# Kernel tuning notes

Measured on AMD Instinct MI355X. Metric: run time of the kernel, lower is better.

Reference implementation:

```python
import jax, jax.numpy as jnp
from jax import lax
import numpy as np

B, T, IN, H, L, C = 1024, 64, 64, 512, 8, 128


def setup_inputs() -> dict:
    key = jax.random.key(0)
    ks = jax.random.split(key, 11)
    s_in = 1.0 / np.sqrt(H)
    return {
        "x": jax.random.normal(ks[0], (B, T, IN), jnp.float32),
        "w_ih0": jax.random.normal(ks[1], (4 * H, IN), jnp.float32) * s_in,
        "w_hh0": jax.random.normal(ks[2], (4 * H, H), jnp.float32) * s_in,
        "b_ih0": jax.random.normal(ks[3], (4 * H,), jnp.float32) * s_in,
        "b_hh0": jax.random.normal(ks[4], (4 * H,), jnp.float32) * s_in,
        "w_ih": jax.random.normal(ks[5], (L - 1, 4 * H, H), jnp.float32) * s_in,
        "w_hh": jax.random.normal(ks[6], (L - 1, 4 * H, H), jnp.float32) * s_in,
        "b_ih": jax.random.normal(ks[7], (L - 1, 4 * H), jnp.float32) * s_in,
        "b_hh": jax.random.normal(ks[8], (L - 1, 4 * H), jnp.float32) * s_in,
        "fc_w": jax.random.normal(ks[9], (C, H * T), jnp.float32) * (1.0 / np.sqrt(H * T)),
        "fc_b": jax.random.normal(ks[10], (C,), jnp.float32) * 0.01,
    }


def _lstm_layer(x_tbd, wi, wh, bi, bh):
    # x_tbd: [T, B, D_in]; returns hidden sequence [T, B, H]
    b = x_tbd.shape[1]
    h_dim = wh.shape[1]
    bias = bi + bh

    def step(carry, x_t):
        h, c = carry
        gates = x_t @ wi.T + h @ wh.T + bias  # [B, 4H]
        i, f, g, o = jnp.split(gates, 4, axis=-1)  # PyTorch gate order i,f,g,o
        i = jax.nn.sigmoid(i)
        f = jax.nn.sigmoid(f)
        g = jnp.tanh(g)
        o = jax.nn.sigmoid(o)
        c = f * c + i * g
        h = o * jnp.tanh(c)
        return (h, c), h

    h0 = jnp.zeros((b, h_dim), x_tbd.dtype)
    _, hs = lax.scan(step, (h0, h0), x_tbd)
    return hs


def reference(x, w_ih0, w_hh0, b_ih0, b_hh0, w_ih, w_hh, b_ih, b_hh, fc_w, fc_b):
    xt = jnp.transpose(x, (1, 0, 2))  # [T, B, IN]
    h = _lstm_layer(xt, w_ih0, w_hh0, b_ih0, b_hh0)
    for l in range(w_ih.shape[0]):  # fixed small layer count
        h = _lstm_layer(h, w_ih[l], w_hh[l], b_ih[l], b_hh[l])
    out = jnp.transpose(h, (1, 0, 2)).reshape(x.shape[0], -1)  # [B, T*H]
    return out @ fc_w.T + fc_b
```

## Files before the change

kernel.cpp:

```cpp
#include <hip/hip_runtime.h>
#include <hip/hip_bf16.h>

#define BB   1024
#define TT   64
#define IND  64
#define HH   512
#define G4   2048
#define NLAYER 8
#define NCLS 128
#define KP   1024
#define RS   8
#define SLOT (32 * 1024 * 16)

typedef __bf16 bf16x8 __attribute__((ext_vector_type(8)));
typedef float  f32x4  __attribute__((ext_vector_type(4)));

typedef const __attribute__((address_space(1))) void* as1cvp;
typedef __attribute__((address_space(3))) void* as3vp;

__device__ __forceinline__ void gload16(void* lds, const void* g) {
  __builtin_amdgcn_global_load_lds((as1cvp)g, (as3vp)lds, 16, 0, 0);
}

__device__ __forceinline__ float sigmf(float x) { return 1.f / (1.f + __expf(-x)); }
__device__ __forceinline__ float tanhfast(float x) { return 2.f / (1.f + __expf(-2.f * x)) - 1.f; }

__global__ void cvt_kernel(const float* __restrict__ s, __bf16* __restrict__ d, int n) {
  int i = blockIdx.x * 256 + threadIdx.x;
  if (i < n) d[i] = (__bf16)s[i];
}

__global__ void pack_w(const float* __restrict__ whh0, const float* __restrict__ wih0,
                       const float* __restrict__ whh, const float* __restrict__ wih,
                       __bf16* __restrict__ Wp) {
  int i = blockIdx.x * 256 + threadIdx.x;
  int k = i & (KP - 1), n = (i >> 10) & 2047, l = i >> 21;
  float v;
  if (k < 512) v = (l == 0) ? whh0[n * 512 + k] : whh[((size_t)(l - 1) * G4 + n) * 512 + k];
  else if (l == 0) v = (k < 512 + IND) ? wih0[n * IND + (k - 512)] : 0.f;
  else v = wih[((size_t)(l - 1) * G4 + n) * 512 + (k - 512)];
  Wp[i] = (__bf16)v;
}

__global__ void bias_prep(const float* __restrict__ bi0, const float* __restrict__ bh0,
                          const float* __restrict__ bi, const float* __restrict__ bh,
                          float* __restrict__ biasb) {
  int i = blockIdx.x * 256 + threadIdx.x;
  int l = i >> 11, k = i & 2047;
  float v = (l == 0) ? (bi0[k] + bh0[k]) : (bi[(l - 1) * G4 + k] + bh[(l - 1) * G4 + k]);
  biasb[i] = v;
}

__global__ void zero_u32(unsigned* __restrict__ p, int n) {
  int i = blockIdx.x * 256 + threadIdx.x;
  if (i < n) p[i] = 0u;
}

__global__ __launch_bounds__(256, 2) void lstm_all(
    const float* __restrict__ xf,
    const __bf16* __restrict__ Wp,
    const float* __restrict__ biasb,
    __bf16* __restrict__ hring,
    __bf16* __restrict__ h7,
    unsigned* __restrict__ flags,
    unsigned* __restrict__ xslot) {
  extern __shared__ __bf16 Wlds[];
  __shared__ int sbs;
  const int tid = threadIdx.x;

  if (tid == 0) {
    unsigned xcc;
    asm volatile("s_getreg_b32 %0, hwreg(HW_REG_XCC_ID)" : "=s"(xcc));
    xcc &= 7u;
    unsigned slot = __hip_atomic_fetch_add(xslot + xcc, 1u, __ATOMIC_RELAXED,
                                           __HIP_MEMORY_SCOPE_AGENT) & 63u;
    sbs = (int)((xcc << 6) | slot);
  }
  __syncthreads();
  const int l  = sbs >> 6;
  const int bx = (sbs >> 5) & 1;
  const int by = sbs & 31;
  const int j0 = by << 4;
  const __bf16* Wl = Wp + (size_t)l * G4 * KP;

  for (int it = 0; it < 16; ++it) {
    const int p = it * 256 + tid;
    const int kt = p >> 8;
    const int q = p & 255;
    const int u = q >> 2;
    const int g = (q & 3) ^ ((u >> 1) & 3);
    const int n = ((u >> 4) << 9) + j0 + (u & 15);
    gload16(&Wlds[p * 8], Wl + (size_t)n * KP + kt * 32 + g * 8);
  }

  const int lane = tid & 63, wv = tid >> 6;
  const int qr = lane >> 4, ml = lane & 15;
  const __bf16* wb[4];
  float bv[4];
  int wsw[4];
#pragma unroll
  for (int g = 0; g < 4; ++g) {
    const int n = g * 512 + j0 + ml;
    wb[g] = Wl + (size_t)n * KP + 512 + qr * 8;
    bv[g] = biasb[l * G4 + n];
    const int u = g * 16 + ml;
    wsw[g] = u * 32 + ((qr ^ ((u >> 1) & 3)) << 3);
  }
  const int r0 = (bx << 9) + (wv << 7);
  const int rowA = r0 + ml;
  const int abase = ((qr >> 1) << 14) + rowA * 16 + ((qr & 1) << 3);
  __bf16* ringL = hring + (size_t)l * RS * SLOT;
  const __bf16* ringU = hring + (size_t)((l > 0 ? l : 1) - 1) * RS * SLOT;
  unsigned* ownf = flags + (l * 2 + bx) * 64;
  unsigned* upf  = flags + ((l > 0 ? l - 1 : 0) * 2 + bx) * 64;
  unsigned* dnf  = flags + ((l < 7 ? l + 1 : 7) * 2 + bx) * 64;
  float c8[8][4] = {};
  __syncthreads();

  for (int t = 0; t < TT; ++t) {
    if (wv == 0) {
      const bool isown = (lane < 32);
      const unsigned* fp = isown ? (ownf + lane) : (upf + (lane - 32));
      const unsigned need = isown ? (unsigned)t : (unsigned)(t + 1);
      const bool act = isown ? (t > 0) : (l > 0);
      for (;;) {
        unsigned v = act ? __hip_atomic_load(fp, __ATOMIC_RELAXED,
                                             __HIP_MEMORY_SCOPE_AGENT)
                         : need;
        if (__all((int)(v >= need))) break;
        __builtin_amdgcn_s_sleep(1);
      }
    }
    __syncthreads();
    if (t > 0 && (t & (RS - 1)) == 0)
      __builtin_amdgcn_fence(__ATOMIC_ACQUIRE, "agent");

    f32x4 acc[8][4];
#pragma unroll
    for (int m = 0; m < 8; ++m)
#pragma unroll
      for (int g = 0; g < 4; ++g)
#pragma unroll
        for (int r = 0; r < 4; ++r) acc[m][g][r] = bv[g];

    if (l == 0) {
#pragma unroll
      for (int m = 0; m < 8; ++m) {
        const float* xr = xf + ((size_t)(rowA + m * 16) * TT + t) * IND + qr * 8;
        const f32x4 f0 = *(const f32x4*)xr;
        const f32x4 f1 = *(const f32x4*)(xr + 4);
        const f32x4 f2 = *(const f32x4*)(xr + 32);
        const f32x4 f3 = *(const f32x4*)(xr + 36);
        bf16x8 a0, a1;
#pragma unroll
        for (int r = 0; r < 4; ++r) {
          a0[r] = (__bf16)f0[r]; a0[4 + r] = (__bf16)f1[r];
          a1[r] = (__bf16)f2[r]; a1[4 + r] = (__bf16)f3[r];
        }
#pragma unroll
        for (int g = 0; g < 4; ++g) {
          acc[m][g] = __builtin_amdgcn_mfma_f32_16x16x32_bf16(
              a0, *(const bf16x8*)(wb[g]), acc[m][g], 0, 0, 0);
          acc[m][g] = __builtin_amdgcn_mfma_f32_16x16x32_bf16(
              a1, *(const bf16x8*)(wb[g] + 32), acc[m][g], 0, 0, 0);
        }
      }
    } else {
      const __bf16* src = ringU + (size_t)(t & (RS - 1)) * SLOT + abase;
      bf16x8 A0[4], A1[4], Wr[2][4];
#pragma unroll
      for (int m = 0; m < 4; ++m) A0[m] = *(const bf16x8*)(src + m * 256);
#pragma unroll
      for (int m = 0; m < 4; ++m) A1[m] = *(const bf16x8*)(src + (4 + m) * 256);
#pragma unroll
      for (int g = 0; g < 4; ++g) Wr[0][g] = *(const bf16x8*)(wb[g]);
#pragma unroll
      for (int kt = 0; kt < 16; ++kt) {
        const __bf16* aknx = src + (kt + 1) * 32768;
#pragma unroll
        for (int m = 0; m < 4; ++m)
#pragma unroll
          for (int g = 0; g < 4; ++g)
            acc[m][g] = __builtin_amdgcn_mfma_f32_16x16x32_bf16(
                A0[m], Wr[kt & 1][g], acc[m][g], 0, 0, 0);
        if (kt < 15) {
#pragma unroll
          for (int m = 0; m < 4; ++m) A0[m] = *(const bf16x8*)(aknx + m * 256);
#pragma unroll
          for (int g = 0; g < 4; ++g)
            Wr[(kt + 1) & 1][g] = *(const bf16x8*)(wb[g] + (kt + 1) * 32);
        }
        __builtin_amdgcn_sched_barrier(0);
#pragma unroll
        for (int m = 0; m < 4; ++m)
#pragma unroll
          for (int g = 0; g < 4; ++g)
            acc[4 + m][g] = __builtin_amdgcn_mfma_f32_16x16x32_bf16(
                A1[m], Wr[kt & 1][g], acc[4 + m][g], 0, 0, 0);
        if (kt < 15) {
#pragma unroll
          for (int m = 0; m < 4; ++m) A1[m] = *(const bf16x8*)(aknx + (4 + m) * 256);
        }
        __builtin_amdgcn_sched_barrier(0);
      }
    }

    if (t > 0) {
      const __bf16* srcH = ((l < 7) ? ringL + (size_t)((t - 1) & (RS - 1)) * SLOT
                                    : h7 + (size_t)(t - 1) * SLOT) + abase;
      bf16x8 A0[4], A1[4];
#pragma unroll
      for (int m = 0; m < 4; ++m) A0[m] = *(const bf16x8*)(srcH + m * 256);
#pragma unroll
      for (int m = 0; m < 4; ++m) A1[m] = *(const bf16x8*)(srcH + (4 + m) * 256);
#pragma unroll
      for (int kt = 0; kt < 16; ++kt) {
        const __bf16* aknx = srcH + (kt + 1) * 32768;
        bf16x8 wf[4];
#pragma unroll
        for (int g = 0; g < 4; ++g) wf[g] = *(const bf16x8*)&Wlds[kt * 2048 + wsw[g]];
#pragma unroll
        for (int m = 0; m < 4; ++m)
#pragma unroll
          for (int g = 0; g < 4; ++g)
            acc[m][g] = __builtin_amdgcn_mfma_f32_16x16x32_bf16(
                A0[m], wf[g], acc[m][g], 0, 0, 0);
        if (kt < 15) {
#pragma unroll
          for (int m = 0; m < 4; ++m) A0[m] = *(const bf16x8*)(aknx + m * 256);
        }
        __builtin_amdgcn_sched_barrier(0);
#pragma unroll
        for (int m = 0; m < 4; ++m)
#pragma unroll
          for (int g = 0; g < 4; ++g)
            acc[4 + m][g] = __builtin_amdgcn_mfma_f32_16x16x32_bf16(
                A1[m], wf[g], acc[4 + m][g], 0, 0, 0);
        if (kt < 15) {
#pragma unroll
          for (int m = 0; m < 4; ++m) A1[m] = *(const bf16x8*)(aknx + (4 + m) * 256);
        }
        __builtin_amdgcn_sched_barrier(0);
      }
    }

    if (wv == 0 && l < 7 && t >= RS) {
      const unsigned need = (unsigned)(t - (RS - 1));
      for (;;) {
        unsigned v = (lane < 32) ? __hip_atomic_load(dnf + lane, __ATOMIC_RELAXED,
                                                     __HIP_MEMORY_SCOPE_AGENT)
                                 : need;
        if (__all((int)(v >= need))) break;
        __builtin_amdgcn_s_sleep(1);
      }
    }
    __syncthreads();

    unsigned short* dst = (unsigned short*)(((l < 7)
        ? ringL + (size_t)(t & (RS - 1)) * SLOT
        : h7 + (size_t)t * SLOT) + ((size_t)by << 14)) + ml;
#pragma unroll
    for (int m = 0; m < 8; ++m) {
      const int rbm = r0 + m * 16 + (qr << 2);
#pragma unroll
      for (int r = 0; r < 4; ++r) {
        const float gi = sigmf(acc[m][0][r]);
        const float gf = sigmf(acc[m][1][r]);
        const float gg = tanhfast(acc[m][2][r]);
        const float go = sigmf(acc[m][3][r]);
        const float cv = gf * c8[m][r] + gi * gg;
        c8[m][r] = cv;
        const __bf16 hv = (__bf16)(go * tanhfast(cv));
        __hip_atomic_store(dst + (size_t)(rbm + r) * 16,
                           __builtin_bit_cast(unsigned short, hv),
                           __ATOMIC_RELAXED, __HIP_MEMORY_SCOPE_AGENT);
      }
    }
    __syncthreads();
    if (tid == 0)
      __hip_atomic_store(ownf + by, (unsigned)(t + 1), __ATOMIC_RELAXED,
                         __HIP_MEMORY_SCOPE_AGENT);
  }
}

__global__ __launch_bounds__(256, 2) void fc_kernel(
    const __bf16* __restrict__ hseq, const __bf16* __restrict__ fcw,
    float* __restrict__ partial) {
  __shared__ __bf16 At[64 * 32];
  __shared__ __bf16 Wt[128 * 32];
  const int tid = threadIdx.x;
  const int b0 = blockIdx.x * 64;
  const int kbase = blockIdx.y * 2048;
  const int lane = tid & 63, wv = tid >> 6;
  const int qr = lane >> 4, ml = lane & 15;
  const int wr = (wv >> 1) * 32, wc = (wv & 1) * 64;
  const int sr = tid >> 2, sk = (tid & 3) * 8;

  f32x4 acc[2][4];
  for (int i = 0; i < 2; i++)
    for (int j = 0; j < 4; j++)
      for (int r = 0; r < 4; r++) acc[i][j][r] = 0.f;

  for (int kt = 0; kt < 64; ++kt) {
    const int k = kbase + kt * 32;
    const int t = k >> 9;
    const int kk = (k & 511) + sk;
    gload16(&At[tid * 8],
            hseq + (size_t)t * SLOT + ((size_t)(kk >> 4) * 1024 + b0 + sr) * 16 + (kk & 15));
    gload16(&Wt[tid * 8],        fcw + (size_t)sr * (TT * HH) + k + sk);
    gload16(&Wt[2048 + tid * 8], fcw + (size_t)(sr + 64) * (TT * HH) + k + sk);
    __syncthreads();
    bf16x8 af[2], bfr[4];
    for (int i = 0; i < 2; i++) af[i]  = *(const bf16x8*)&At[(wr + i * 16 + ml) * 32 + qr * 8];
    for (int j = 0; j < 4; j++) bfr[j] = *(const bf16x8*)&Wt[(wc + j * 16 + ml) * 32 + qr * 8];
    for (int i = 0; i < 2; i++)
      for (int j = 0; j < 4; j++)
        acc[i][j] = __builtin_amdgcn_mfma_f32_16x16x32_bf16(af[i], bfr[j], acc[i][j], 0, 0, 0);
    __syncthreads();
  }
  for (int i = 0; i < 2; i++)
    for (int j = 0; j < 4; j++)
      for (int r = 0; r < 4; r++)
        partial[((size_t)blockIdx.y * BB + b0 + wr + i * 16 + qr * 4 + r) * NCLS + wc + j * 16 + ml] =
            acc[i][j][r];
}

__global__ void fc_reduce(const float* __restrict__ partial, const float* __restrict__ fcb,
                          float* __restrict__ out) {
  int i = blockIdx.x * 256 + threadIdx.x;
  float s = fcb[i & 127];
  for (int p = 0; p < 16; p++) s += partial[(size_t)p * (BB * NCLS) + i];
  out[i] = s;
}

extern "C" void kernel_launch(void* const* d_in, const int* in_sizes, int n_in,
                              void* d_out, int out_size, void* d_ws, size_t ws_size,
                              hipStream_t stream) {
  const float* x    = (const float*)d_in[0];
  const float* wih0 = (const float*)d_in[1];
  const float* whh0 = (const float*)d_in[2];
  const float* bih0 = (const float*)d_in[3];
  const float* bhh0 = (const float*)d_in[4];
  const float* wih  = (const float*)d_in[5];
  const float* whh  = (const float*)d_in[6];
  const float* bih  = (const float*)d_in[7];
  const float* bhh  = (const float*)d_in[8];
  const float* fcw  = (const float*)d_in[9];
  const float* fcb  = (const float*)d_in[10];
  float* out = (float*)d_out;

  hipFuncSetAttribute((const void*)lstm_all,
                      hipFuncAttributeMaxDynamicSharedMemorySize, 65536);

  size_t off = 0;
  char* base = (char*)d_ws;
  auto carve = [&](size_t bytes) -> char* {
    char* p = base + off;
    off += (bytes + 255) & ~(size_t)255;
    return p;
  };
  __bf16*   Wp    = (__bf16*)carve((size_t)NLAYER * G4 * KP * 2);
  __bf16*   fcwb  = (__bf16*)carve((size_t)NCLS * TT * HH * 2);
  float*    biasb = (float*)carve((size_t)NLAYER * G4 * 4);
  __bf16*   hring = (__bf16*)carve((size_t)7 * RS * SLOT * 2);
  __bf16*   h7    = (__bf16*)carve((size_t)TT * SLOT * 2);
  float*    part  = (float*)carve((size_t)16 * BB * NCLS * 4);
  unsigned* flags = (unsigned*)carve((size_t)(NLAYER * 2 * 64 + 64) * 4);
  unsigned* xslot = flags + NLAYER * 2 * 64;

  pack_w<<<(NLAYER * G4 * KP) / 256, 256, 0, stream>>>(whh0, wih0, whh, wih, Wp);
  cvt_kernel<<<(NCLS * TT * HH) / 256, 256, 0, stream>>>(fcw, fcwb, NCLS * TT * HH);
  bias_prep<<<(NLAYER * G4) / 256, 256, 0, stream>>>(bih0, bhh0, bih, bhh, biasb);
  zero_u32<<<(NLAYER * 2 * 64 + 64 + 255) / 256, 256, 0, stream>>>(
      flags, NLAYER * 2 * 64 + 64);

  lstm_all<<<512, 256, 65536, stream>>>(x, Wp, biasb, hring, h7, flags, xslot);

  fc_kernel<<<dim3(16, 16), 256, 0, stream>>>(h7, fcwb, part);
  fc_reduce<<<(BB * NCLS) / 256, 256, 0, stream>>>(part, fcb, out);
}
```

Measured before the change: 4.292 ms.

## Compute next step's input projection before waiting on own-layer hidden state

Restructures the per-timestep loop so the input-to-hidden MFMA work for step t+1 runs right after publishing h_t, instead of after waiting for every peer block's h_t. The goal is to take the input projection off the recurrent critical path, so the wait on sibling blocks overlaps with useful work. The upstream-layer flag wait also moves to just before that early projection. This adds an extra barrier per step and changes the order of flag waits, which could shift pipeline dependencies between layers.

```diff
diff --git a/kernel.cpp b/kernel.cpp
--- a/kernel.cpp
+++ b/kernel.cpp
@@ -115,18 +115,143 @@
   unsigned* upf  = flags + ((l > 0 ? l - 1 : 0) * 2 + bx) * 64;
   unsigned* dnf  = flags + ((l < 7 ? l + 1 : 7) * 2 + bx) * 64;
   float c8[8][4] = {};
+  f32x4 acc[8][4];
   __syncthreads();
 
+  auto initAcc = [&]() {
+#pragma unroll
+    for (int m = 0; m < 8; ++m)
+#pragma unroll
+      for (int g = 0; g < 4; ++g)
+#pragma unroll
+        for (int r = 0; r < 4; ++r) acc[m][g][r] = bv[g];
+  };
+
+  auto xpartL0 = [&](int tx) {
+#pragma unroll
+    for (int m = 0; m < 8; ++m) {
+      const float* xr = xf + ((size_t)(rowA + m * 16) * TT + tx) * IND + qr * 8;
+      const f32x4 f0 = *(const f32x4*)xr;
+      const f32x4 f1 = *(const f32x4*)(xr + 4);
+      const f32x4 f2 = *(const f32x4*)(xr + 32);
+      const f32x4 f3 = *(const f32x4*)(xr + 36);
+      bf16x8 a0, a1;
+#pragma unroll
+      for (int r = 0; r < 4; ++r) {
+        a0[r] = (__bf16)f0[r]; a0[4 + r] = (__bf16)f1[r];
+        a1[r] = (__bf16)f2[r]; a1[4 + r] = (__bf16)f3[r];
+      }
+#pragma unroll
+      for (int g = 0; g < 4; ++g) {
+        acc[m][g] = __builtin_amdgcn_mfma_f32_16x16x32_bf16(
+            a0, *(const bf16x8*)(wb[g]), acc[m][g], 0, 0, 0);
+        acc[m][g] = __builtin_amdgcn_mfma_f32_16x16x32_bf16(
+            a1, *(const bf16x8*)(wb[g] + 32), acc[m][g], 0, 0, 0);
+      }
+    }
+  };
+
+  auto xpartL = [&](int tx) {
+    const __bf16* src = ringU + (size_t)(tx & (RS - 1)) * SLOT + abase;
+    bf16x8 A0[4], A1[4], Wr[2][4];
+#pragma unroll
+    for (int m = 0; m < 4; ++m) A0[m] = *(const bf16x8*)(src + m * 256);
+#pragma unroll
+    for (int m = 0; m < 4; ++m) A1[m] = *(const bf16x8*)(src + (4 + m) * 256);
+#pragma unroll
+    for (int g = 0; g < 4; ++g) Wr[0][g] = *(const bf16x8*)(wb[g]);
+#pragma unroll
+    for (int kt = 0; kt < 16; ++kt) {
+      const __bf16* aknx = src + (kt + 1) * 32768;
+#pragma unroll
+      for (int m = 0; m < 4; ++m)
+#pragma unroll
+        for (int g = 0; g < 4; ++g)
+          acc[m][g] = __builtin_amdgcn_mfma_f32_16x16x32_bf16(
+              A0[m], Wr[kt & 1][g], acc[m][g], 0, 0, 0);
+      if (kt < 15) {
+#pragma unroll
+        for (int m = 0; m < 4; ++m) A0[m] = *(const bf16x8*)(aknx + m * 256);
+#pragma unroll
+        for (int g = 0; g < 4; ++g)
+          Wr[(kt + 1) & 1][g] = *(const bf16x8*)(wb[g] + (kt + 1) * 32);
+      }
+      __builtin_amdgcn_sched_barrier(0);
+#pragma unroll
+      for (int m = 0; m < 4; ++m)
+#pragma unroll
+        for (int g = 0; g < 4; ++g)
+          acc[4 + m][g] = __builtin_amdgcn_mfma_f32_16x16x32_bf16(
+              A1[m], Wr[kt & 1][g], acc[4 + m][g], 0, 0, 0);
+      if (kt < 15) {
+#pragma unroll
+        for (int m = 0; m < 4; ++m) A1[m] = *(const bf16x8*)(aknx + (4 + m) * 256);
+      }
+      __builtin_amdgcn_sched_barrier(0);
+    }
+  };
+
+  auto hpart = [&](int t) {
+    const __bf16* srcH = ((l < 7) ? ringL + (size_t)((t - 1) & (RS - 1)) * SLOT
+                                  : h7 + (size_t)(t - 1) * SLOT) + abase;
+    bf16x8 A0[4], A1[4];
+#pragma unroll
+    for (int m = 0; m < 4; ++m) A0[m] = *(const bf16x8*)(srcH + m * 256);
+#pragma unroll
+    for (int m = 0; m < 4; ++m) A1[m] = *(const bf16x8*)(srcH + (4 + m) * 256);
+#pragma unroll
+    for (int kt = 0; kt < 16; ++kt) {
+      const __bf16* aknx = srcH + (kt + 1) * 32768;
+      bf16x8 wf[4];
+#pragma unroll
+      for (int g = 0; g < 4; ++g) wf[g] = *(const bf16x8*)&Wlds[kt * 2048 + wsw[g]];
+#pragma unroll
+      for (int m = 0; m < 4; ++m)
+#pragma unroll
+        for (int g = 0; g < 4; ++g)
+          acc[m][g] = __builtin_amdgcn_mfma_f32_16x16x32_bf16(
+              A0[m], wf[g], acc[m][g], 0, 0, 0);
+      if (kt < 15) {
+#pragma unroll
+        for (int m = 0; m < 4; ++m) A0[m] = *(const bf16x8*)(aknx + m * 256);
+      }
+      __builtin_amdgcn_sched_barrier(0);
+#pragma unroll
+      for (int m = 0; m < 4; ++m)
+#pragma unroll
+        for (int g = 0; g < 4; ++g)
+          acc[4 + m][g] = __builtin_amdgcn_mfma_f32_16x16x32_bf16(
+              A1[m], wf[g], acc[4 + m][g], 0, 0, 0);
+      if (kt < 15) {
+#pragma unroll
+        for (int m = 0; m < 4; ++m) A1[m] = *(const bf16x8*)(aknx + (4 + m) * 256);
+      }
+      __builtin_amdgcn_sched_barrier(0);
+    }
+  };
+
+  if (l > 0) {
+    if (wv == 0) {
+      for (;;) {
+        unsigned v = (lane < 32) ? __hip_atomic_load(upf + lane, __ATOMIC_RELAXED,
+                                                     __HIP_MEMORY_SCOPE_AGENT)
+                                 : 1u;
+        if (__all((int)(v >= 1u))) break;
+        __builtin_amdgcn_s_sleep(1);
+      }
+    }
+    __syncthreads();
+  }
+  initAcc();
+  if (l == 0) xpartL0(0); else xpartL(0);
+
   for (int t = 0; t < TT; ++t) {
-    if (wv == 0) {
-      const bool isown = (lane < 32);
-      const unsigned* fp = isown ? (ownf + lane) : (upf + (lane - 32));
-      const unsigned need = isown ? (unsigned)t : (unsigned)(t + 1);
-      const bool act = isown ? (t > 0) : (l > 0);
+    if (wv == 0 && t > 0) {
+      const unsigned need = (unsigned)t;
       for (;;) {
-        unsigned v = act ? __hip_atomic_load(fp, __ATOMIC_RELAXED,
-                                             __HIP_MEMORY_SCOPE_AGENT)
-                         : need;
+        unsigned v = (lane < 32) ? __hip_atomic_load(ownf + lane, __ATOMIC_RELAXED,
+                                                     __HIP_MEMORY_SCOPE_AGENT)
+                                 : need;
         if (__all((int)(v >= need))) break;
         __builtin_amdgcn_s_sleep(1);
       }
@@ -135,114 +260,7 @@
     if (t > 0 && (t & (RS - 1)) == 0)
       __builtin_amdgcn_fence(__ATOMIC_ACQUIRE, "agent");
 
-    f32x4 acc[8][4];
-#pragma unroll
-    for (int m = 0; m < 8; ++m)
-#pragma unroll
-      for (int g = 0; g < 4; ++g)
-#pragma unroll
-        for (int r = 0; r < 4; ++r) acc[m][g][r] = bv[g];
-
-    if (l == 0) {
-#pragma unroll
-      for (int m = 0; m < 8; ++m) {
-        const float* xr = xf + ((size_t)(rowA + m * 16) * TT + t) * IND + qr * 8;
-        const f32x4 f0 = *(const f32x4*)xr;
-        const f32x4 f1 = *(const f32x4*)(xr + 4);
-        const f32x4 f2 = *(const f32x4*)(xr + 32);
-        const f32x4 f3 = *(const f32x4*)(xr + 36);
-        bf16x8 a0, a1;
-#pragma unroll
-        for (int r = 0; r < 4; ++r) {
-          a0[r] = (__bf16)f0[r]; a0[4 + r] = (__bf16)f1[r];
-          a1[r] = (__bf16)f2[r]; a1[4 + r] = (__bf16)f3[r];
-        }
-#pragma unroll
-        for (int g = 0; g < 4; ++g) {
-          acc[m][g] = __builtin_amdgcn_mfma_f32_16x16x32_bf16(
-              a0, *(const bf16x8*)(wb[g]), acc[m][g], 0, 0, 0);
-          acc[m][g] = __builtin_amdgcn_mfma_f32_16x16x32_bf16(
-              a1, *(const bf16x8*)(wb[g] + 32), acc[m][g], 0, 0, 0);
-        }
-      }
-    } else {
-      const __bf16* src = ringU + (size_t)(t & (RS - 1)) * SLOT + abase;
-      bf16x8 A0[4], A1[4], Wr[2][4];
-#pragma unroll
-      for (int m = 0; m < 4; ++m) A0[m] = *(const bf16x8*)(src + m * 256);
-#pragma unroll
-      for (int m = 0; m < 4; ++m) A1[m] = *(const bf16x8*)(src + (4 + m) * 256);
-#pragma unroll
-      for (int g = 0; g < 4; ++g) Wr[0][g] = *(const bf16x8*)(wb[g]);
-#pragma unroll
-      for (int kt = 0; kt < 16; ++kt) {
-        const __bf16* aknx = src + (kt + 1) * 32768;
-#pragma unroll
-        for (int m = 0; m < 4; ++m)
-#pragma unroll
-          for (int g = 0; g < 4; ++g)
-            acc[m][g] = __builtin_amdgcn_mfma_f32_16x16x32_bf16(
-                A0[m], Wr[kt & 1][g], acc[m][g], 0, 0, 0);
-        if (kt < 15) {
-#pragma unroll
-          for (int m = 0; m < 4; ++m) A0[m] = *(const bf16x8*)(aknx + m * 256);
-#pragma unroll
-          for (int g = 0; g < 4; ++g)
-            Wr[(kt + 1) & 1][g] = *(const bf16x8*)(wb[g] + (kt + 1) * 32);
-        }
-        __builtin_amdgcn_sched_barrier(0);
-#pragma unroll
-        for (int m = 0; m < 4; ++m)
-#pragma unroll
-          for (int g = 0; g < 4; ++g)
-            acc[4 + m][g] = __builtin_amdgcn_mfma_f32_16x16x32_bf16(
-                A1[m], Wr[kt & 1][g], acc[4 + m][g], 0, 0, 0);
-        if (kt < 15) {
-#pragma unroll
-          for (int m = 0; m < 4; ++m) A1[m] = *(const bf16x8*)(aknx + (4 + m) * 256);
-        }
-        __builtin_amdgcn_sched_barrier(0);
-      }
-    }
-
-    if (t > 0) {
-      const __bf16* srcH = ((l < 7) ? ringL + (size_t)((t - 1) & (RS - 1)) * SLOT
-                                    : h7 + (size_t)(t - 1) * SLOT) + abase;
-      bf16x8 A0[4], A1[4];
-#pragma unroll
-      for (int m = 0; m < 4; ++m) A0[m] = *(const bf16x8*)(srcH + m * 256);
-#pragma unroll
-      for (int m = 0; m < 4; ++m) A1[m] = *(const bf16x8*)(srcH + (4 + m) * 256);
-#pragma unroll
-      for (int kt = 0; kt < 16; ++kt) {
-        const __bf16* aknx = srcH + (kt + 1) * 32768;
-        bf16x8 wf[4];
-#pragma unroll
-        for (int g = 0; g < 4; ++g) wf[g] = *(const bf16x8*)&Wlds[kt * 2048 + wsw[g]];
-#pragma unroll
-        for (int m = 0; m < 4; ++m)
-#pragma unroll
-          for (int g = 0; g < 4; ++g)
-            acc[m][g] = __builtin_amdgcn_mfma_f32_16x16x32_bf16(
-                A0[m], wf[g], acc[m][g], 0, 0, 0);
-        if (kt < 15) {
-#pragma unroll
-          for (int m = 0; m < 4; ++m) A0[m] = *(const bf16x8*)(aknx + m * 256);
-        }
-        __builtin_amdgcn_sched_barrier(0);
-#pragma unroll
-        for (int m = 0; m < 4; ++m)
-#pragma unroll
-          for (int g = 0; g < 4; ++g)
-            acc[4 + m][g] = __builtin_amdgcn_mfma_f32_16x16x32_bf16(
-                A1[m], wf[g], acc[4 + m][g], 0, 0, 0);
-        if (kt < 15) {
-#pragma unroll
-          for (int m = 0; m < 4; ++m) A1[m] = *(const bf16x8*)(aknx + (4 + m) * 256);
-        }
-        __builtin_amdgcn_sched_barrier(0);
-      }
-    }
+    if (t > 0) hpart(t);
 
     if (wv == 0 && l < 7 && t >= RS) {
       const unsigned need = (unsigned)(t - (RS - 1));
@@ -280,6 +298,24 @@
     if (tid == 0)
       __hip_atomic_store(ownf + by, (unsigned)(t + 1), __ATOMIC_RELAXED,
                          __HIP_MEMORY_SCOPE_AGENT);
+
+    if (t + 1 < TT) {
+      if (l > 0) {
+        if (wv == 0) {
+          const unsigned need = (unsigned)(t + 2);
+          for (;;) {
+            unsigned v = (lane < 32) ? __hip_atomic_load(upf + lane, __ATOMIC_RELAXED,
+                                                         __HIP_MEMORY_SCOPE_AGENT)
+                                     : need;
+            if (__all((int)(v >= need))) break;
+            __builtin_amdgcn_s_sleep(1);
+          }
+        }
+        __syncthreads();
+      }
+      initAcc();
+      if (l == 0) xpartL0(t + 1); else xpartL(t + 1);
+    }
   }
 }
 
```

Result: faster. 3.643 ms (-15.1%).

## Use per-wave flags and hoist next-step input projection before recurrent wait

Applied to the files above, without the earlier changes.

Replaces the block-wide barrier and single-wave flag polling with per-wavefront flags. Each wave polls only the producer waves whose rows it consumes and publishes its own progress after a vmcnt wait. The input-projection GEMM for step t+1 is computed right after step t's h is written, so it runs while the recurrent dependency from other blocks is still resolving. The cost is four times as many flag polls and stores, and correctness now rests on per-wave ordering and memory visibility instead of __syncthreads.

```diff
diff --git a/kernel.cpp b/kernel.cpp
--- a/kernel.cpp
+++ b/kernel.cpp
@@ -111,150 +111,150 @@
   const int abase = ((qr >> 1) << 14) + rowA * 16 + ((qr & 1) << 3);
   __bf16* ringL = hring + (size_t)l * RS * SLOT;
   const __bf16* ringU = hring + (size_t)((l > 0 ? l : 1) - 1) * RS * SLOT;
-  unsigned* ownf = flags + (l * 2 + bx) * 64;
-  unsigned* upf  = flags + ((l > 0 ? l - 1 : 0) * 2 + bx) * 64;
-  unsigned* dnf  = flags + ((l < 7 ? l + 1 : 7) * 2 + bx) * 64;
+  unsigned* ownfw = flags + ((l * 2 + bx) * 4 + wv) * 32;
+  unsigned* upfw  = flags + (((l > 0 ? l - 1 : 0) * 2 + bx) * 4 + wv) * 32;
+  unsigned* dnfw  = flags + (((l < 7 ? l + 1 : 7) * 2 + bx) * 4 + wv) * 32;
   float c8[8][4] = {};
+  f32x4 acc[8][4];
   __syncthreads();
 
+  auto pollge = [&](const unsigned* fp, unsigned need) {
+    for (;;) {
+      unsigned v = (lane < 32) ? __hip_atomic_load(fp + lane, __ATOMIC_RELAXED,
+                                                   __HIP_MEMORY_SCOPE_AGENT)
+                               : need;
+      if (__all((int)(v >= need))) break;
+      __builtin_amdgcn_s_sleep(1);
+    }
+    asm volatile("" ::: "memory");
+    __builtin_amdgcn_sched_barrier(0);
+  };
+
+  auto initAcc = [&]() {
+#pragma unroll
+    for (int m = 0; m < 8; ++m)
+#pragma unroll
+      for (int g = 0; g < 4; ++g)
+#pragma unroll
+        for (int r = 0; r < 4; ++r) acc[m][g][r] = bv[g];
+  };
+
+  auto xpartL0 = [&](int tx) {
+#pragma unroll
+    for (int m = 0; m < 8; ++m) {
+      const float* xr = xf + ((size_t)(rowA + m * 16) * TT + tx) * IND + qr * 8;
+      const f32x4 f0 = *(const f32x4*)xr;
+      const f32x4 f1 = *(const f32x4*)(xr + 4);
+      const f32x4 f2 = *(const f32x4*)(xr + 32);
+      const f32x4 f3 = *(const f32x4*)(xr + 36);
+      bf16x8 a0, a1;
+#pragma unroll
+      for (int r = 0; r < 4; ++r) {
+        a0[r] = (__bf16)f0[r]; a0[4 + r] = (__bf16)f1[r];
+        a1[r] = (__bf16)f2[r]; a1[4 + r] = (__bf16)f3[r];
+      }
+#pragma unroll
+      for (int g = 0; g < 4; ++g) {
+        acc[m][g] = __builtin_amdgcn_mfma_f32_16x16x32_bf16(
+            a0, *(const bf16x8*)(wb[g]), acc[m][g], 0, 0, 0);
+        acc[m][g] = __builtin_amdgcn_mfma_f32_16x16x32_bf16(
+            a1, *(const bf16x8*)(wb[g] + 32), acc[m][g], 0, 0, 0);
+      }
+    }
+  };
+
+  auto xpartL = [&](int tx) {
+    const __bf16* src = ringU + (size_t)(tx & (RS - 1)) * SLOT + abase;
+    bf16x8 A0[4], A1[4], Wr[2][4];
+#pragma unroll
+    for (int m = 0; m < 4; ++m) A0[m] = *(const bf16x8*)(src + m * 256);
+#pragma unroll
+    for (int m = 0; m < 4; ++m) A1[m] = *(const bf16x8*)(src + (4 + m) * 256);
+#pragma unroll
+    for (int g = 0; g < 4; ++g) Wr[0][g] = *(const bf16x8*)(wb[g]);
+#pragma unroll
+    for (int kt = 0; kt < 16; ++kt) {
+      const __bf16* aknx = src + (kt + 1) * 32768;
+#pragma unroll
+      for (int m = 0; m < 4; ++m)
+#pragma unroll
+        for (int g = 0; g < 4; ++g)
+          acc[m][g] = __builtin_amdgcn_mfma_f32_16x16x32_bf16(
+              A0[m], Wr[kt & 1][g], acc[m][g], 0, 0, 0);
+      if (kt < 15) {
+#pragma unroll
+        for (int m = 0; m < 4; ++m) A0[m] = *(const bf16x8*)(aknx + m * 256);
+#pragma unroll
+        for (int g = 0; g < 4; ++g)
+          Wr[(kt + 1) & 1][g] = *(const bf16x8*)(wb[g] + (kt + 1) * 32);
+      }
+      __builtin_amdgcn_sched_barrier(0);
+#pragma unroll
+      for (int m = 0; m < 4; ++m)
+#pragma unroll
+        for (int g = 0; g < 4; ++g)
+          acc[4 + m][g] = __builtin_amdgcn_mfma_f32_16x16x32_bf16(
+              A1[m], Wr[kt & 1][g], acc[4 + m][g], 0, 0, 0);
+      if (kt < 15) {
+#pragma unroll
+        for (int m = 0; m < 4; ++m) A1[m] = *(const bf16x8*)(aknx + (4 + m) * 256);
+      }
+      __builtin_amdgcn_sched_barrier(0);
+    }
+  };
+
+  auto hpart = [&](int t) {
+    const __bf16* srcH = ((l < 7) ? ringL + (size_t)((t - 1) & (RS - 1)) * SLOT
+                                  : h7 + (size_t)(t - 1) * SLOT) + abase;
+    bf16x8 A0[4], A1[4];
+#pragma unroll
+    for (int m = 0; m < 4; ++m) A0[m] = *(const bf16x8*)(srcH + m * 256);
+#pragma unroll
+    for (int m = 0; m < 4; ++m) A1[m] = *(const bf16x8*)(srcH + (4 + m) * 256);
+#pragma unroll
+    for (int kt = 0; kt < 16; ++kt) {
+      const __bf16* aknx = srcH + (kt + 1) * 32768;
+      bf16x8 wf[4];
+#pragma unroll
+      for (int g = 0; g < 4; ++g) wf[g] = *(const bf16x8*)&Wlds[kt * 2048 + wsw[g]];
+#pragma unroll
+      for (int m = 0; m < 4; ++m)
+#pragma unroll
+        for (int g = 0; g < 4; ++g)
+          acc[m][g] = __builtin_amdgcn_mfma_f32_16x16x32_bf16(
+              A0[m], wf[g], acc[m][g], 0, 0, 0);
+      if (kt < 15) {
+#pragma unroll
+        for (int m = 0; m < 4; ++m) A0[m] = *(const bf16x8*)(aknx + m * 256);
+      }
+      __builtin_amdgcn_sched_barrier(0);
+#pragma unroll
+      for (int m = 0; m < 4; ++m)
+#pragma unroll
+        for (int g = 0; g < 4; ++g)
+          acc[4 + m][g] = __builtin_amdgcn_mfma_f32_16x16x32_bf16(
+              A1[m], wf[g], acc[4 + m][g], 0, 0, 0);
+      if (kt < 15) {
+#pragma unroll
+        for (int m = 0; m < 4; ++m) A1[m] = *(const bf16x8*)(aknx + (4 + m) * 256);
+      }
+      __builtin_amdgcn_sched_barrier(0);
+    }
+  };
+
+  if (l > 0) pollge(upfw, 1u);
+  initAcc();
+  if (l == 0) xpartL0(0); else xpartL(0);
+
   for (int t = 0; t < TT; ++t) {
-    if (wv == 0) {
-      const bool isown = (lane < 32);
-      const unsigned* fp = isown ? (ownf + lane) : (upf + (lane - 32));
-      const unsigned need = isown ? (unsigned)t : (unsigned)(t + 1);
-      const bool act = isown ? (t > 0) : (l > 0);
-      for (;;) {
-        unsigned v = act ? __hip_atomic_load(fp, __ATOMIC_RELAXED,
-                                             __HIP_MEMORY_SCOPE_AGENT)
-                         : need;
-        if (__all((int)(v >= need))) break;
-        __builtin_amdgcn_s_sleep(1);
-      }
-    }
-    __syncthreads();
-    if (t > 0 && (t & (RS - 1)) == 0)
-      __builtin_amdgcn_fence(__ATOMIC_ACQUIRE, "agent");
-
-    f32x4 acc[8][4];
-#pragma unroll
-    for (int m = 0; m < 8; ++m)
-#pragma unroll
-      for (int g = 0; g < 4; ++g)
-#pragma unroll
-        for (int r = 0; r < 4; ++r) acc[m][g][r] = bv[g];
-
-    if (l == 0) {
-#pragma unroll
-      for (int m = 0; m < 8; ++m) {
-        const float* xr = xf + ((size_t)(rowA + m * 16) * TT + t) * IND + qr * 8;
-        const f32x4 f0 = *(const f32x4*)xr;
-        const f32x4 f1 = *(const f32x4*)(xr + 4);
-        const f32x4 f2 = *(const f32x4*)(xr + 32);
-        const f32x4 f3 = *(const f32x4*)(xr + 36);
-        bf16x8 a0, a1;
-#pragma unroll
-        for (int r = 0; r < 4; ++r) {
-          a0[r] = (__bf16)f0[r]; a0[4 + r] = (__bf16)f1[r];
-          a1[r] = (__bf16)f2[r]; a1[4 + r] = (__bf16)f3[r];
-        }
-#pragma unroll
-        for (int g = 0; g < 4; ++g) {
-          acc[m][g] = __builtin_amdgcn_mfma_f32_16x16x32_bf16(
-              a0, *(const bf16x8*)(wb[g]), acc[m][g], 0, 0, 0);
-          acc[m][g] = __builtin_amdgcn_mfma_f32_16x16x32_bf16(
-              a1, *(const bf16x8*)(wb[g] + 32), acc[m][g], 0, 0, 0);
-        }
-      }
-    } else {
-      const __bf16* src = ringU + (size_t)(t & (RS - 1)) * SLOT + abase;
-      bf16x8 A0[4], A1[4], Wr[2][4];
-#pragma unroll
-      for (int m = 0; m < 4; ++m) A0[m] = *(const bf16x8*)(src + m * 256);
-#pragma unroll
-      for (int m = 0; m < 4; ++m) A1[m] = *(const bf16x8*)(src + (4 + m) * 256);
-#pragma unroll
-      for (int g = 0; g < 4; ++g) Wr[0][g] = *(const bf16x8*)(wb[g]);
-#pragma unroll
-      for (int kt = 0; kt < 16; ++kt) {
-        const __bf16* aknx = src + (kt + 1) * 32768;
-#pragma unroll
-        for (int m = 0; m < 4; ++m)
-#pragma unroll
-          for (int g = 0; g < 4; ++g)
-            acc[m][g] = __builtin_amdgcn_mfma_f32_16x16x32_bf16(
-                A0[m], Wr[kt & 1][g], acc[m][g], 0, 0, 0);
-        if (kt < 15) {
-#pragma unroll
-          for (int m = 0; m < 4; ++m) A0[m] = *(const bf16x8*)(aknx + m * 256);
-#pragma unroll
-          for (int g = 0; g < 4; ++g)
-            Wr[(kt + 1) & 1][g] = *(const bf16x8*)(wb[g] + (kt + 1) * 32);
-        }
-        __builtin_amdgcn_sched_barrier(0);
-#pragma unroll
-        for (int m = 0; m < 4; ++m)
-#pragma unroll
-          for (int g = 0; g < 4; ++g)
-            acc[4 + m][g] = __builtin_amdgcn_mfma_f32_16x16x32_bf16(
-                A1[m], Wr[kt & 1][g], acc[4 + m][g], 0, 0, 0);
-        if (kt < 15) {
-#pragma unroll
-          for (int m = 0; m < 4; ++m) A1[m] = *(const bf16x8*)(aknx + (4 + m) * 256);
-        }
-        __builtin_amdgcn_sched_barrier(0);
-      }
-    }
-
     if (t > 0) {
-      const __bf16* srcH = ((l < 7) ? ringL + (size_t)((t - 1) & (RS - 1)) * SLOT
-                                    : h7 + (size_t)(t - 1) * SLOT) + abase;
-      bf16x8 A0[4], A1[4];
-#pragma unroll
-      for (int m = 0; m < 4; ++m) A0[m] = *(const bf16x8*)(srcH + m * 256);
-#pragma unroll
-      for (int m = 0; m < 4; ++m) A1[m] = *(const bf16x8*)(srcH + (4 + m) * 256);
-#pragma unroll
-      for (int kt = 0; kt < 16; ++kt) {
-        const __bf16* aknx = srcH + (kt + 1) * 32768;
-        bf16x8 wf[4];
-#pragma unroll
-        for (int g = 0; g < 4; ++g) wf[g] = *(const bf16x8*)&Wlds[kt * 2048 + wsw[g]];
-#pragma unroll
-        for (int m = 0; m < 4; ++m)
-#pragma unroll
-          for (int g = 0; g < 4; ++g)
-            acc[m][g] = __builtin_amdgcn_mfma_f32_16x16x32_bf16(
-                A0[m], wf[g], acc[m][g], 0, 0, 0);
-        if (kt < 15) {
-#pragma unroll
-          for (int m = 0; m < 4; ++m) A0[m] = *(const bf16x8*)(aknx + m * 256);
-        }
-        __builtin_amdgcn_sched_barrier(0);
-#pragma unroll
-        for (int m = 0; m < 4; ++m)
-#pragma unroll
-          for (int g = 0; g < 4; ++g)
-            acc[4 + m][g] = __builtin_amdgcn_mfma_f32_16x16x32_bf16(
-                A1[m], wf[g], acc[4 + m][g], 0, 0, 0);
-        if (kt < 15) {
-#pragma unroll
-          for (int m = 0; m < 4; ++m) A1[m] = *(const bf16x8*)(aknx + (4 + m) * 256);
-        }
-        __builtin_amdgcn_sched_barrier(0);
-      }
-    }
-
-    if (wv == 0 && l < 7 && t >= RS) {
-      const unsigned need = (unsigned)(t - (RS - 1));
-      for (;;) {
-        unsigned v = (lane < 32) ? __hip_atomic_load(dnf + lane, __ATOMIC_RELAXED,
-                                                     __HIP_MEMORY_SCOPE_AGENT)
-                                 : need;
-        if (__all((int)(v >= need))) break;
-        __builtin_amdgcn_s_sleep(1);
-      }
-    }
-    __syncthreads();
+      pollge(ownfw, (unsigned)t);
+      if ((t & (RS - 1)) == 0)
+        __builtin_amdgcn_fence(__ATOMIC_ACQUIRE, "agent");
+      hpart(t);
+    }
+
+    if (l < 7 && t >= RS) pollge(dnfw, (unsigned)(t - (RS - 1)));
 
     unsigned short* dst = (unsigned short*)(((l < 7)
         ? ringL + (size_t)(t & (RS - 1)) * SLOT
@@ -276,10 +276,17 @@
                            __ATOMIC_RELAXED, __HIP_MEMORY_SCOPE_AGENT);
       }
     }
-    __syncthreads();
-    if (tid == 0)
-      __hip_atomic_store(ownf + by, (unsigned)(t + 1), __ATOMIC_RELAXED,
+    asm volatile("s_waitcnt vmcnt(0)" ::: "memory");
+    __builtin_amdgcn_sched_barrier(0);
+    if (lane == 0)
+      __hip_atomic_store(ownfw + by, (unsigned)(t + 1), __ATOMIC_RELAXED,
                          __HIP_MEMORY_SCOPE_AGENT);
+
+    if (t + 1 < TT) {
+      if (l > 0) pollge(upfw, (unsigned)(t + 2));
+      initAcc();
+      if (l == 0) xpartL0(t + 1); else xpartL(t + 1);
+    }
   }
 }
 
@@ -365,14 +372,14 @@
   __bf16*   hring = (__bf16*)carve((size_t)7 * RS * SLOT * 2);
   __bf16*   h7    = (__bf16*)carve((size_t)TT * SLOT * 2);
   float*    part  = (float*)carve((size_t)16 * BB * NCLS * 4);
-  unsigned* flags = (unsigned*)carve((size_t)(NLAYER * 2 * 64 + 64) * 4);
-  unsigned* xslot = flags + NLAYER * 2 * 64;
+  unsigned* flags = (unsigned*)carve((size_t)(NLAYER * 2 * 4 * 32 + 64) * 4);
+  unsigned* xslot = flags + NLAYER * 2 * 4 * 32;
 
   pack_w<<<(NLAYER * G4 * KP) / 256, 256, 0, stream>>>(whh0, wih0, whh, wih, Wp);
   cvt_kernel<<<(NCLS * TT * HH) / 256, 256, 0, stream>>>(fcw, fcwb, NCLS * TT * HH);
   bias_prep<<<(NLAYER * G4) / 256, 256, 0, stream>>>(bih0, bhh0, bih, bhh, biasb);
-  zero_u32<<<(NLAYER * 2 * 64 + 64 + 255) / 256, 256, 0, stream>>>(
-      flags, NLAYER * 2 * 64 + 64);
+  zero_u32<<<(NLAYER * 2 * 4 * 32 + 64 + 255) / 256, 256, 0, stream>>>(
+      flags, NLAYER * 2 * 4 * 32 + 64);
 
   lstm_all<<<512, 256, 65536, stream>>>(x, Wp, biasb, hring, h7, flags, xslot);
 
```

New measurement: 3.687 ms. 14.1% less time.
